# Performance work log

Hardware: AMD Instinct MI355X
Metric: run time of the kernel (lower is better)

Reference implementation:

```python
import jax, jax.numpy as jnp
import numpy as np

N = 4096
NFEAT = 256
NHID1 = 64
NHID2 = 32
NCLASS = 8
NHEADS = 4
NADJ = 2
ALPHA = 0.2  # leaky relu slope
NEG = -9e15


def setup_inputs() -> dict:
    key = jax.random.key(0)
    ks = jax.random.split(key, 14)
    x = jax.random.normal(ks[0], (N, NFEAT), jnp.float32)
    adj = (jax.random.uniform(ks[1], (NADJ, N, N)) < 0.01).astype(jnp.float32)
    adj = jnp.maximum(adj, jnp.eye(N, dtype=jnp.float32)[None])
    s = 0.05
    W1 = jax.random.normal(ks[2], (NADJ, NHEADS, NFEAT, NHID1), jnp.float32) * s
    a1 = jax.random.normal(ks[3], (NADJ, NHEADS, 2, NHID1), jnp.float32) * s
    W2 = jax.random.normal(ks[4], (NADJ, NHEADS, NHID1, NHID2), jnp.float32) * s
    a2 = jax.random.normal(ks[5], (NADJ, NHEADS, 2, NHID2), jnp.float32) * s
    Wi1 = jax.random.normal(ks[6], (NHID1 * NHEADS, NHID1), jnp.float32) * s
    bi1 = jnp.zeros((NHID1,), jnp.float32)
    Wi2 = jax.random.normal(ks[7], (NHID2 * NHEADS, NCLASS), jnp.float32) * s
    bi2 = jnp.zeros((NCLASS,), jnp.float32)
    Wf = jax.random.normal(ks[8], (NCLASS * NADJ, NCLASS), jnp.float32) * s
    bf = jnp.zeros((NCLASS,), jnp.float32)
    return {"x": x, "adj": adj, "W1": W1, "a1": a1, "W2": W2, "a2": a2,
            "Wi1": Wi1, "bi1": bi1, "Wi2": Wi2, "bi2": bi2, "Wf": Wf, "bf": bf}


def gat_multihead(x, adj_i, W, a):
    # x: [n, f]; adj_i: [n, n]; W: [h, f, o]; a: [h, 2, o]
    Wh = jnp.einsum('nf,hfo->hno', x, W)                 # [h, n, o]
    f_src = jnp.einsum('hno,ho->hn', Wh, a[:, 0])        # [h, n]
    f_dst = jnp.einsum('hno,ho->hn', Wh, a[:, 1])        # [h, n]
    e = jax.nn.leaky_relu(f_src[:, :, None] + f_dst[:, None, :], ALPHA)
    e = jnp.where(adj_i[None] > 0, e, NEG)               # masked scores [h, n, n]
    att = jax.nn.softmax(e, axis=-1)
    h = jnp.einsum('hnm,hmo->hno', att, Wh)              # aggregate
    h = jax.nn.elu(h)                                     # concat=True -> elu
    n = x.shape[0]
    return jnp.transpose(h, (1, 0, 2)).reshape(n, -1)     # [n, h*o]


def reference(x, adj, W1, a1, W2, a2, Wi1, bi1, Wi2, bi2, Wf, bf):
    outs = []
    for i in range(NADJ):  # small fixed loop over adjacency graphs
        xi = gat_multihead(x, adj[i], W1[i], a1[i])
        xi = jax.nn.elu(xi @ Wi1 + bi1)
        xi = gat_multihead(xi, adj[i], W2[i], a2[i])
        xi = jax.nn.elu(xi @ Wi2 + bi2)
        outs.append(xi)
    out = jnp.concatenate(outs, axis=1) @ Wf + bf         # [n, nclass]
    l1_loss = jnp.mean(jnp.abs(Wf))
    return jax.nn.log_softmax(out, axis=1), l1_loss
```

## Files before the change

kernel.cpp:

```cpp
#include <hip/hip_runtime.h>
#include <hip/hip_bf16.h>

#define NN 4096
#define NFEAT 256
#define NHID1 64
#define NHID2 32
#define NCLASS 8
#define NHEADS 4
#define NADJ 2
#define CAP 128

template <int KDIM, int NDIM, int RPTY, int ACT, int COEF>
__device__ __forceinline__ void gemm_body(
    const float* __restrict__ A, const float* __restrict__ B,
    const float* __restrict__ bias, float* __restrict__ C,
    const float* __restrict__ ag, float* __restrict__ fsrc,
    float* __restrict__ fdst, const int row0b,
    float* __restrict__ sA, float* __restrict__ sB) {
  constexpr int KT = 32;
  constexpr int TX = NDIM / 4;
  constexpr int TY = 256 / TX;
  constexpr int BR = TY * RPTY;
  constexpr int LDA = BR + 4;
  constexpr int LDB = NDIM + 4;
  const int tid = threadIdx.x;
  const int tx = tid % TX, ty = tid / TX;
  const int c0 = tx * 4;
  float acc[RPTY][4];
#pragma unroll
  for (int i = 0; i < RPTY; ++i)
#pragma unroll
    for (int j = 0; j < 4; ++j) acc[i][j] = 0.f;

  for (int kt = 0; kt < KDIM; kt += KT) {
    __syncthreads();
    for (int i = tid; i < BR * (KT / 4); i += 256) {
      const int r = i / (KT / 4), e = i % (KT / 4);
      const float4 v = *(const float4*)(A + (size_t)(row0b + r) * KDIM + kt + e * 4);
      sA[(e * 4 + 0) * LDA + r] = v.x;
      sA[(e * 4 + 1) * LDA + r] = v.y;
      sA[(e * 4 + 2) * LDA + r] = v.z;
      sA[(e * 4 + 3) * LDA + r] = v.w;
    }
    for (int i = tid; i < KT * (NDIM / 4); i += 256) {
      const int k = i / (NDIM / 4), cc = i % (NDIM / 4);
      *(float4*)&sB[k * LDB + cc * 4] = *(const float4*)(B + (size_t)(kt + k) * NDIM + cc * 4);
    }
    __syncthreads();
#pragma unroll
    for (int k = 0; k < KT; ++k) {
      float a4[RPTY];
      if constexpr (RPTY == 4) {
        const float4 t = *(const float4*)&sA[k * LDA + ty * 4];
        a4[0] = t.x; a4[1] = t.y; a4[2] = t.z; a4[3] = t.w;
      } else {
        const float2 t = *(const float2*)&sA[k * LDA + ty * 2];
        a4[0] = t.x; a4[1] = t.y;
      }
      const float4 bv = *(const float4*)&sB[k * LDB + c0];
      const float b4[4] = {bv.x, bv.y, bv.z, bv.w};
#pragma unroll
      for (int i = 0; i < RPTY; ++i)
#pragma unroll
        for (int j = 0; j < 4; ++j) acc[i][j] += a4[i] * b4[j];
    }
  }
  float b4[4] = {0.f, 0.f, 0.f, 0.f};
  if (bias) {
    const float4 bb = *(const float4*)&bias[c0];
    b4[0] = bb.x; b4[1] = bb.y; b4[2] = bb.z; b4[3] = bb.w;
  }
#pragma unroll
  for (int i = 0; i < RPTY; ++i) {
    const int row = row0b + ty * RPTY + i;
    float4 o;
    float* op = (float*)&o;
#pragma unroll
    for (int j = 0; j < 4; ++j) {
      float v = acc[i][j] + b4[j];
      if (ACT == 1) v = v > 0.f ? v : (__expf(v) - 1.f);
      op[j] = v;
    }
    *(float4*)&C[(size_t)row * NDIM + c0] = o;
  }
  if constexpr (COEF) {
    float aS[4], aD[4];
#pragma unroll
    for (int j = 0; j < 4; ++j) { aS[j] = ag[c0 + j]; aD[j] = ag[NDIM + c0 + j]; }
#pragma unroll
    for (int i = 0; i < RPTY; ++i) {
      float s = 0.f, d = 0.f;
#pragma unroll
      for (int j = 0; j < 4; ++j) { s += acc[i][j] * aS[j]; d += acc[i][j] * aD[j]; }
#pragma unroll
      for (int off = TX / 2; off; off >>= 1) {
        s += __shfl_xor(s, off);
        d += __shfl_xor(d, off);
      }
      if (tx == 0) {
        const int row = row0b + ty * RPTY + i;
        fsrc[row] = s;
        fdst[row] = d;
      }
    }
  }
}

__global__ __launch_bounds__(256) void k1_gemm_edges(
    const float* __restrict__ x, const float* __restrict__ W1,
    const float* __restrict__ a1, float* __restrict__ Wh1,
    float* __restrict__ fs1, float* __restrict__ fd1,
    const float* __restrict__ adj, int* __restrict__ eidx,
    int* __restrict__ ecnt) {
  __shared__ float sA[32 * (64 + 4)];
  __shared__ float sB[32 * (64 + 4)];
  constexpr int NB_GEMM = (NN / 64) * NHEADS * NADJ;
  if (blockIdx.x < NB_GEMM) {
    int b = blockIdx.x;
    const int tile = b % (NN / 64); b /= (NN / 64);
    const int h = b % NHEADS;
    const int g = b / NHEADS;
    const int gh = g * NHEADS + h;
    gemm_body<NFEAT, NHID1, 4, 0, 1>(
        x, W1 + (size_t)gh * NFEAT * NHID1, nullptr,
        Wh1 + (size_t)gh * NN * NHID1, a1 + (size_t)gh * 2 * NHID1,
        fs1 + (size_t)gh * NN, fd1 + (size_t)gh * NN, tile * 64, sA, sB);
  } else {
    const int wave = threadIdx.x >> 6;
    const int lane = threadIdx.x & 63;
    const int r = (blockIdx.x - NB_GEMM) * 4 + wave;
    const float4* row = (const float4*)(adj + (size_t)r * NN);
    int* out = eidx + (size_t)r * CAP;
    int base = 0;
    for (int c = 0; c < NN; c += 256) {
      const float4 v = row[(c >> 2) + lane];
      const int j0 = c + lane * 4;
      const float vt[4] = {v.x, v.y, v.z, v.w};
#pragma unroll
      for (int t = 0; t < 4; ++t) {
        const bool hit = vt[t] > 0.f;
        const unsigned long long m = __ballot(hit);
        if (hit) {
          const int pos = base + __popcll(m & ((1ull << lane) - 1ull));
          if (pos < CAP) out[pos] = j0 + t;
        }
        base += __popcll(m);
      }
    }
    if (lane == 0) ecnt[r] = base < CAP ? base : CAP;
  }
}

template <int KDIM, int NDIM, int RPTY, int ACT, int COEF>
__global__ __launch_bounds__(256) void gemm_tile(
    const float* __restrict__ A, const float* __restrict__ B,
    const float* __restrict__ bias, float* __restrict__ C,
    const float* __restrict__ av, float* __restrict__ fsrc,
    float* __restrict__ fdst,
    size_t asG, size_t bsH, size_t bsG, size_t csH, size_t csG) {
  constexpr int TX = NDIM / 4;
  constexpr int TY = 256 / TX;
  constexpr int BR = TY * RPTY;
  __shared__ float sA[32 * (BR + 4)];
  __shared__ float sB[32 * (NDIM + 4)];
  const int g = blockIdx.z, h = blockIdx.y;
  const int gh = g * NHEADS + h;
  gemm_body<KDIM, NDIM, RPTY, ACT, COEF>(
      A + (size_t)g * asG, B + (size_t)g * bsG + (size_t)h * bsH, bias,
      C + (size_t)g * csG + (size_t)h * csH,
      COEF ? av + (size_t)gh * 2 * NDIM : nullptr,
      COEF ? fsrc + (size_t)gh * NN : nullptr,
      COEF ? fdst + (size_t)gh * NN : nullptr,
      (int)blockIdx.x * BR, sA, sB);
}

#define GATHER(ACC, JJ)                                                     \
  do {                                                                      \
    const float w_ = wgt[wave][JJ];                                         \
    const float4 v_ = *(const float4*)(Wh + (size_t)midx[wave][JJ] * O + c4); \
    ACC.x += w_ * v_.x; ACC.y += w_ * v_.y;                                 \
    ACC.z += w_ * v_.z; ACC.w += w_ * v_.w;                                 \
  } while (0)

template <int O>
__global__ __launch_bounds__(256) void aggregate(const float* __restrict__ Wh,
                                                 const float* __restrict__ fsrc,
                                                 const float* __restrict__ fdst,
                                                 const int* __restrict__ eidx,
                                                 const int* __restrict__ ecnt,
                                                 float* __restrict__ Hout) {
  constexpr int CPL = O / 4;
  constexpr int EPW = 64 / CPL;
  __shared__ float wgt[4][CAP];
  __shared__ int midx[4][CAP];
  const int wave = threadIdx.x >> 6;
  const int lane = threadIdx.x & 63;
  const int n = blockIdx.x * 4 + wave;
  const int h = blockIdx.y, g = blockIdx.z;
  const int gh = g * NHEADS + h;
  Wh += (size_t)gh * NN * O;
  const int cnt = ecnt[(size_t)g * NN + n];
  const int* ei = eidx + (size_t)(g * NN + n) * CAP;
  const float fs = fsrc[(size_t)gh * NN + n];
  const float* fd = fdst + (size_t)gh * NN;
  float mx = -3.4e38f;
  for (int j = lane; j < cnt; j += 64) {
    const int m = ei[j];
    float e = fs + fd[m];
    e = e > 0.f ? e : 0.2f * e;
    midx[wave][j] = m;
    wgt[wave][j] = e;
    mx = fmaxf(mx, e);
  }
  for (int off = 32; off; off >>= 1) mx = fmaxf(mx, __shfl_xor(mx, off));
  float sm = 0.f;
  for (int j = lane; j < cnt; j += 64) {
    const float w = __expf(wgt[wave][j] - mx);
    wgt[wave][j] = w;
    sm += w;
  }
  for (int off = 32; off; off >>= 1) sm += __shfl_xor(sm, off);
  const int sub = lane / CPL;
  const int c4 = (lane % CPL) * 4;
  float4 a0 = {0, 0, 0, 0}, a1 = {0, 0, 0, 0}, a2 = {0, 0, 0, 0}, a3 = {0, 0, 0, 0};
  int j = sub;
  for (; j + 3 * EPW < cnt; j += 4 * EPW) {
    GATHER(a0, j);
    GATHER(a1, j + EPW);
    GATHER(a2, j + 2 * EPW);
    GATHER(a3, j + 3 * EPW);
  }
  for (; j < cnt; j += EPW) GATHER(a0, j);
  float4 acc;
  acc.x = (a0.x + a1.x) + (a2.x + a3.x);
  acc.y = (a0.y + a1.y) + (a2.y + a3.y);
  acc.z = (a0.z + a1.z) + (a2.z + a3.z);
  acc.w = (a0.w + a1.w) + (a2.w + a3.w);
#pragma unroll
  for (int off = CPL; off < 64; off <<= 1) {
    acc.x += __shfl_xor(acc.x, off);
    acc.y += __shfl_xor(acc.y, off);
    acc.z += __shfl_xor(acc.z, off);
    acc.w += __shfl_xor(acc.w, off);
  }
  if (lane < CPL) {
    const float inv = 1.f / sm;
    float4 o;
    o.x = acc.x * inv; o.y = acc.y * inv; o.z = acc.z * inv; o.w = acc.w * inv;
    o.x = o.x > 0.f ? o.x : (__expf(o.x) - 1.f);
    o.y = o.y > 0.f ? o.y : (__expf(o.y) - 1.f);
    o.z = o.z > 0.f ? o.z : (__expf(o.z) - 1.f);
    o.w = o.w > 0.f ? o.w : (__expf(o.w) - 1.f);
    *(float4*)&Hout[(size_t)g * NN * (NHEADS * O) + (size_t)n * (NHEADS * O) +
                    h * O + c4] = o;
  }
}

__global__ __launch_bounds__(256) void tail_fused(const float* __restrict__ h2,
                                                  const float* __restrict__ Wi2,
                                                  const float* __restrict__ bi2,
                                                  const float* __restrict__ Wf,
                                                  const float* __restrict__ bfv,
                                                  float* __restrict__ out) {
  constexpr int K = NHEADS * NHID2;
  __shared__ float A0[16][K + 4];
  __shared__ float A1[16][K + 4];
  __shared__ float Bs[K][NCLASS];
  __shared__ float WfS[2 * NCLASS][NCLASS];
  __shared__ float cat[16][2 * NCLASS + 1];
  const int tid = threadIdx.x;
  const int row0 = blockIdx.x * 16;
  for (int i = tid; i < 16 * (K / 4); i += 256) {
    const int r = i >> 5, e = i & 31;
    *(float4*)&A0[r][e * 4] = *(const float4*)(h2 + (size_t)(row0 + r) * K + e * 4);
    *(float4*)&A1[r][e * 4] =
        *(const float4*)(h2 + (size_t)NN * K + (size_t)(row0 + r) * K + e * 4);
  }
  ((float4*)Bs)[tid] = ((const float4*)Wi2)[tid];
  if (tid < 32) ((float4*)WfS)[tid] = ((const float4*)Wf)[tid];
  __syncthreads();
  const int c = tid & 7;
  const int kk = (tid >> 3) & 1;
  const int r = tid >> 4;
  float s0 = kk ? 0.f : bi2[c], s1 = kk ? 0.f : bi2[c];
#pragma unroll 8
  for (int k = kk * (K / 2); k < (kk + 1) * (K / 2); ++k) {
    s0 += A0[r][k] * Bs[k][c];
    s1 += A1[r][k] * Bs[k][c];
  }
  s0 += __shfl_xor(s0, 8);
  s1 += __shfl_xor(s1, 8);
  if (kk == 0) {
    cat[r][c] = s0 > 0.f ? s0 : (__expf(s0) - 1.f);
    cat[r][NCLASS + c] = s1 > 0.f ? s1 : (__expf(s1) - 1.f);
  }
  __syncthreads();
  float logit = bfv[c];
#pragma unroll
  for (int k = 0; k < 2 * NCLASS; ++k) logit += cat[r][k] * WfS[k][c];
  float m = logit;
#pragma unroll
  for (int off = 4; off; off >>= 1) m = fmaxf(m, __shfl_xor(m, off));
  float s = __expf(logit - m);
#pragma unroll
  for (int off = 4; off; off >>= 1) s += __shfl_xor(s, off);
  if (kk == 0) out[(size_t)(row0 + r) * NCLASS + c] = logit - (logf(s) + m);
  if (blockIdx.x == 0 && tid < 64) {
    float v = fabsf(Wf[tid]) + fabsf(Wf[64 + tid]);
    for (int off = 32; off; off >>= 1) v += __shfl_xor(v, off);
    if (tid == 0) out[NN * NCLASS] = v * (1.f / (2 * NCLASS * NCLASS));
  }
}

extern "C" void kernel_launch(void* const* d_in, const int* in_sizes, int n_in,
                              void* d_out, int out_size, void* d_ws, size_t ws_size,
                              hipStream_t stream) {
  const float* x = (const float*)d_in[0];
  const float* adj = (const float*)d_in[1];
  const float* W1 = (const float*)d_in[2];
  const float* a1 = (const float*)d_in[3];
  const float* W2 = (const float*)d_in[4];
  const float* a2 = (const float*)d_in[5];
  const float* Wi1 = (const float*)d_in[6];
  const float* bi1 = (const float*)d_in[7];
  const float* Wi2 = (const float*)d_in[8];
  const float* bi2 = (const float*)d_in[9];
  const float* Wf = (const float*)d_in[10];
  const float* bfv = (const float*)d_in[11];
  float* out = (float*)d_out;

  char* ws = (char*)d_ws;
  int* eidx = (int*)ws;     ws += (size_t)NADJ * NN * CAP * 4;
  int* ecnt = (int*)ws;     ws += (size_t)NADJ * NN * 4;
  float* Wh1 = (float*)ws;  ws += (size_t)NADJ * NHEADS * NN * NHID1 * 4;
  float* fs1 = (float*)ws;  ws += (size_t)NADJ * NHEADS * NN * 4;
  float* fd1 = (float*)ws;  ws += (size_t)NADJ * NHEADS * NN * 4;
  float* h1 = (float*)ws;   ws += (size_t)NADJ * NN * NHEADS * NHID1 * 4;
  float* x1 = (float*)ws;   ws += (size_t)NADJ * NN * NHID1 * 4;
  float* Wh2 = (float*)ws;  ws += (size_t)NADJ * NHEADS * NN * NHID2 * 4;
  float* fs2 = (float*)ws;  ws += (size_t)NADJ * NHEADS * NN * 4;
  float* fd2 = (float*)ws;  ws += (size_t)NADJ * NHEADS * NN * 4;
  float* h2 = (float*)ws;   ws += (size_t)NADJ * NN * NHEADS * NHID2 * 4;

  k1_gemm_edges<<<512 + NADJ * NN / 4, 256, 0, stream>>>(
      x, W1, a1, Wh1, fs1, fd1, adj, eidx, ecnt);

  aggregate<NHID1><<<dim3(NN / 4, NHEADS, NADJ), 256, 0, stream>>>(
      Wh1, fs1, fd1, eidx, ecnt, h1);

  gemm_tile<NHEADS * NHID1, NHID1, 2, 1, 0><<<dim3(NN / 32, 1, NADJ), 256, 0, stream>>>(
      h1, Wi1, bi1, x1, nullptr, nullptr, nullptr,
      (size_t)NN * NHEADS * NHID1, 0, 0, 0, (size_t)NN * NHID1);

  gemm_tile<NHID1, NHID2, 4, 0, 1><<<dim3(NN / 128, NHEADS, NADJ), 256, 0, stream>>>(
      x1, W2, nullptr, Wh2, a2, fs2, fd2,
      (size_t)NN * NHID1, (size_t)NHID1 * NHID2, (size_t)NHEADS * NHID1 * NHID2,
      (size_t)NN * NHID2, (size_t)NHEADS * NN * NHID2);

  aggregate<NHID2><<<dim3(NN / 4, NHEADS, NADJ), 256, 0, stream>>>(
      Wh2, fs2, fd2, eidx, ecnt, h2);

  tail_fused<<<NN / 16, 256, 0, stream>>>(h2, Wi2, bi2, Wf, bfv, out);
}
```

Before: 101.3 us.

## Fuse layer-1 aggregation with both GEMMs, and layer-2 aggregation with the tail

Cuts the pipeline from six launches to three. Layer-1 attention aggregation, the Wi1 projection with ELU, and the W2 projection plus attention coefficients now run in one kernel over 16-row tiles held in shared memory. Layer-2 aggregation for both graphs is fused with the Wi2/Wf tail and log-softmax. This removes the h1, x1 and h2 round trips through global memory and several launch gaps. In exchange, each wave loops over rows and heads serially, the grids are smaller, and k2 uses a large amount of shared memory, so occupancy and parallelism drop.

```diff
diff --git a/kernel.cpp b/kernel.cpp
--- a/kernel.cpp
+++ b/kernel.cpp
@@ -10,12 +10,11 @@
 #define NADJ 2
 #define CAP 128
 
-template <int KDIM, int NDIM, int RPTY, int ACT, int COEF>
+template <int KDIM, int NDIM, int RPTY>
 __device__ __forceinline__ void gemm_body(
     const float* __restrict__ A, const float* __restrict__ B,
-    const float* __restrict__ bias, float* __restrict__ C,
-    const float* __restrict__ ag, float* __restrict__ fsrc,
-    float* __restrict__ fdst, const int row0b,
+    float* __restrict__ C, const float* __restrict__ ag,
+    float* __restrict__ fsrc, float* __restrict__ fdst, const int row0b,
     float* __restrict__ sA, float* __restrict__ sB) {
   constexpr int KT = 32;
   constexpr int TX = NDIM / 4;
@@ -49,14 +48,8 @@
     __syncthreads();
 #pragma unroll
     for (int k = 0; k < KT; ++k) {
-      float a4[RPTY];
-      if constexpr (RPTY == 4) {
-        const float4 t = *(const float4*)&sA[k * LDA + ty * 4];
-        a4[0] = t.x; a4[1] = t.y; a4[2] = t.z; a4[3] = t.w;
-      } else {
-        const float2 t = *(const float2*)&sA[k * LDA + ty * 2];
-        a4[0] = t.x; a4[1] = t.y;
-      }
+      const float4 t = *(const float4*)&sA[k * LDA + ty * 4];
+      const float a4[4] = {t.x, t.y, t.z, t.w};
       const float4 bv = *(const float4*)&sB[k * LDB + c0];
       const float b4[4] = {bv.x, bv.y, bv.z, bv.w};
 #pragma unroll
@@ -64,44 +57,31 @@
 #pragma unroll
         for (int j = 0; j < 4; ++j) acc[i][j] += a4[i] * b4[j];
     }
-  }
-  float b4[4] = {0.f, 0.f, 0.f, 0.f};
-  if (bias) {
-    const float4 bb = *(const float4*)&bias[c0];
-    b4[0] = bb.x; b4[1] = bb.y; b4[2] = bb.z; b4[3] = bb.w;
   }
 #pragma unroll
   for (int i = 0; i < RPTY; ++i) {
     const int row = row0b + ty * RPTY + i;
     float4 o;
-    float* op = (float*)&o;
-#pragma unroll
-    for (int j = 0; j < 4; ++j) {
-      float v = acc[i][j] + b4[j];
-      if (ACT == 1) v = v > 0.f ? v : (__expf(v) - 1.f);
-      op[j] = v;
-    }
+    o.x = acc[i][0]; o.y = acc[i][1]; o.z = acc[i][2]; o.w = acc[i][3];
     *(float4*)&C[(size_t)row * NDIM + c0] = o;
   }
-  if constexpr (COEF) {
-    float aS[4], aD[4];
-#pragma unroll
-    for (int j = 0; j < 4; ++j) { aS[j] = ag[c0 + j]; aD[j] = ag[NDIM + c0 + j]; }
-#pragma unroll
-    for (int i = 0; i < RPTY; ++i) {
-      float s = 0.f, d = 0.f;
-#pragma unroll
-      for (int j = 0; j < 4; ++j) { s += acc[i][j] * aS[j]; d += acc[i][j] * aD[j]; }
-#pragma unroll
-      for (int off = TX / 2; off; off >>= 1) {
-        s += __shfl_xor(s, off);
-        d += __shfl_xor(d, off);
-      }
-      if (tx == 0) {
-        const int row = row0b + ty * RPTY + i;
-        fsrc[row] = s;
-        fdst[row] = d;
-      }
+  float aS[4], aD[4];
+#pragma unroll
+  for (int j = 0; j < 4; ++j) { aS[j] = ag[c0 + j]; aD[j] = ag[NDIM + c0 + j]; }
+#pragma unroll
+  for (int i = 0; i < RPTY; ++i) {
+    float s = 0.f, d = 0.f;
+#pragma unroll
+    for (int j = 0; j < 4; ++j) { s += acc[i][j] * aS[j]; d += acc[i][j] * aD[j]; }
+#pragma unroll
+    for (int off = TX / 2; off; off >>= 1) {
+      s += __shfl_xor(s, off);
+      d += __shfl_xor(d, off);
+    }
+    if (tx == 0) {
+      const int row = row0b + ty * RPTY + i;
+      fsrc[row] = s;
+      fdst[row] = d;
     }
   }
 }
@@ -121,10 +101,10 @@
     const int h = b % NHEADS;
     const int g = b / NHEADS;
     const int gh = g * NHEADS + h;
-    gemm_body<NFEAT, NHID1, 4, 0, 1>(
-        x, W1 + (size_t)gh * NFEAT * NHID1, nullptr,
-        Wh1 + (size_t)gh * NN * NHID1, a1 + (size_t)gh * 2 * NHID1,
-        fs1 + (size_t)gh * NN, fd1 + (size_t)gh * NN, tile * 64, sA, sB);
+    gemm_body<NFEAT, NHID1, 4>(
+        x, W1 + (size_t)gh * NFEAT * NHID1, Wh1 + (size_t)gh * NN * NHID1,
+        a1 + (size_t)gh * 2 * NHID1, fs1 + (size_t)gh * NN,
+        fd1 + (size_t)gh * NN, tile * 64, sA, sB);
   } else {
     const int wave = threadIdx.x >> 6;
     const int lane = threadIdx.x & 63;
@@ -151,164 +131,259 @@
   }
 }
 
-template <int KDIM, int NDIM, int RPTY, int ACT, int COEF>
-__global__ __launch_bounds__(256) void gemm_tile(
-    const float* __restrict__ A, const float* __restrict__ B,
-    const float* __restrict__ bias, float* __restrict__ C,
-    const float* __restrict__ av, float* __restrict__ fsrc,
-    float* __restrict__ fdst,
-    size_t asG, size_t bsH, size_t bsG, size_t csH, size_t csG) {
-  constexpr int TX = NDIM / 4;
-  constexpr int TY = 256 / TX;
-  constexpr int BR = TY * RPTY;
-  __shared__ float sA[32 * (BR + 4)];
-  __shared__ float sB[32 * (NDIM + 4)];
-  const int g = blockIdx.z, h = blockIdx.y;
-  const int gh = g * NHEADS + h;
-  gemm_body<KDIM, NDIM, RPTY, ACT, COEF>(
-      A + (size_t)g * asG, B + (size_t)g * bsG + (size_t)h * bsH, bias,
-      C + (size_t)g * csG + (size_t)h * csH,
-      COEF ? av + (size_t)gh * 2 * NDIM : nullptr,
-      COEF ? fsrc + (size_t)gh * NN : nullptr,
-      COEF ? fdst + (size_t)gh * NN : nullptr,
-      (int)blockIdx.x * BR, sA, sB);
-}
-
-#define GATHER(ACC, JJ)                                                     \
-  do {                                                                      \
-    const float w_ = wgt[wave][JJ];                                         \
-    const float4 v_ = *(const float4*)(Wh + (size_t)midx[wave][JJ] * O + c4); \
-    ACC.x += w_ * v_.x; ACC.y += w_ * v_.y;                                 \
-    ACC.z += w_ * v_.z; ACC.w += w_ * v_.w;                                 \
-  } while (0)
-
-template <int O>
-__global__ __launch_bounds__(256) void aggregate(const float* __restrict__ Wh,
-                                                 const float* __restrict__ fsrc,
-                                                 const float* __restrict__ fdst,
-                                                 const int* __restrict__ eidx,
-                                                 const int* __restrict__ ecnt,
-                                                 float* __restrict__ Hout) {
-  constexpr int CPL = O / 4;
-  constexpr int EPW = 64 / CPL;
+__global__ __launch_bounds__(256) void k2_fused(
+    const float* __restrict__ Wh1, const float* __restrict__ fs1,
+    const float* __restrict__ fd1, const int* __restrict__ eidx,
+    const int* __restrict__ ecnt, const float* __restrict__ Wi1,
+    const float* __restrict__ bi1, const float* __restrict__ W2,
+    const float* __restrict__ a2, float* __restrict__ Wh2,
+    float* __restrict__ fs2, float* __restrict__ fd2) {
+  __shared__ float h1row[16][256];
+  __shared__ float stage[8192];
+  __shared__ float x1row[16][68];
   __shared__ float wgt[4][CAP];
   __shared__ int midx[4][CAP];
+  const int g = blockIdx.y;
+  const int n0 = blockIdx.x * 16;
   const int wave = threadIdx.x >> 6;
   const int lane = threadIdx.x & 63;
-  const int n = blockIdx.x * 4 + wave;
-  const int h = blockIdx.y, g = blockIdx.z;
-  const int gh = g * NHEADS + h;
-  Wh += (size_t)gh * NN * O;
-  const int cnt = ecnt[(size_t)g * NN + n];
-  const int* ei = eidx + (size_t)(g * NN + n) * CAP;
-  const float fs = fsrc[(size_t)gh * NN + n];
-  const float* fd = fdst + (size_t)gh * NN;
-  float mx = -3.4e38f;
-  for (int j = lane; j < cnt; j += 64) {
-    const int m = ei[j];
-    float e = fs + fd[m];
-    e = e > 0.f ? e : 0.2f * e;
-    midx[wave][j] = m;
-    wgt[wave][j] = e;
-    mx = fmaxf(mx, e);
-  }
-  for (int off = 32; off; off >>= 1) mx = fmaxf(mx, __shfl_xor(mx, off));
-  float sm = 0.f;
-  for (int j = lane; j < cnt; j += 64) {
-    const float w = __expf(wgt[wave][j] - mx);
-    wgt[wave][j] = w;
-    sm += w;
-  }
-  for (int off = 32; off; off >>= 1) sm += __shfl_xor(sm, off);
-  const int sub = lane / CPL;
-  const int c4 = (lane % CPL) * 4;
-  float4 a0 = {0, 0, 0, 0}, a1 = {0, 0, 0, 0}, a2 = {0, 0, 0, 0}, a3 = {0, 0, 0, 0};
-  int j = sub;
-  for (; j + 3 * EPW < cnt; j += 4 * EPW) {
-    GATHER(a0, j);
-    GATHER(a1, j + EPW);
-    GATHER(a2, j + 2 * EPW);
-    GATHER(a3, j + 3 * EPW);
-  }
-  for (; j < cnt; j += EPW) GATHER(a0, j);
-  float4 acc;
-  acc.x = (a0.x + a1.x) + (a2.x + a3.x);
-  acc.y = (a0.y + a1.y) + (a2.y + a3.y);
-  acc.z = (a0.z + a1.z) + (a2.z + a3.z);
-  acc.w = (a0.w + a1.w) + (a2.w + a3.w);
-#pragma unroll
-  for (int off = CPL; off < 64; off <<= 1) {
-    acc.x += __shfl_xor(acc.x, off);
-    acc.y += __shfl_xor(acc.y, off);
-    acc.z += __shfl_xor(acc.z, off);
-    acc.w += __shfl_xor(acc.w, off);
-  }
-  if (lane < CPL) {
-    const float inv = 1.f / sm;
-    float4 o;
-    o.x = acc.x * inv; o.y = acc.y * inv; o.z = acc.z * inv; o.w = acc.w * inv;
-    o.x = o.x > 0.f ? o.x : (__expf(o.x) - 1.f);
-    o.y = o.y > 0.f ? o.y : (__expf(o.y) - 1.f);
-    o.z = o.z > 0.f ? o.z : (__expf(o.z) - 1.f);
-    o.w = o.w > 0.f ? o.w : (__expf(o.w) - 1.f);
-    *(float4*)&Hout[(size_t)g * NN * (NHEADS * O) + (size_t)n * (NHEADS * O) +
-                    h * O + c4] = o;
+
+  for (int rr = 0; rr < 4; ++rr) {
+    const int r = wave * 4 + rr;
+    const int n = n0 + r;
+    const int cnt = ecnt[g * NN + n];
+    const int* ei = eidx + (size_t)(g * NN + n) * CAP;
+    for (int j = lane; j < cnt; j += 64) midx[wave][j] = ei[j];
+    for (int h = 0; h < 4; ++h) {
+      const int gh = g * NHEADS + h;
+      const float fsv = fs1[(size_t)gh * NN + n];
+      const float* fdv = fd1 + (size_t)gh * NN;
+      float mx = -3.4e38f;
+      for (int j = lane; j < cnt; j += 64) {
+        float e = fsv + fdv[midx[wave][j]];
+        e = e > 0.f ? e : 0.2f * e;
+        wgt[wave][j] = e;
+        mx = fmaxf(mx, e);
+      }
+      for (int off = 32; off; off >>= 1) mx = fmaxf(mx, __shfl_xor(mx, off));
+      float sm = 0.f;
+      for (int j = lane; j < cnt; j += 64) {
+        const float w = __expf(wgt[wave][j] - mx);
+        wgt[wave][j] = w;
+        sm += w;
+      }
+      for (int off = 32; off; off >>= 1) sm += __shfl_xor(sm, off);
+      const float* WhH = Wh1 + (size_t)gh * NN * NHID1;
+      const int sub = lane >> 4;
+      const int c4 = (lane & 15) * 4;
+      float4 a0 = {0, 0, 0, 0}, a1v = {0, 0, 0, 0}, a2v = {0, 0, 0, 0}, a3 = {0, 0, 0, 0};
+#define GAT1(ACC, JJ)                                                        \
+  {                                                                          \
+    const float w_ = wgt[wave][JJ];                                          \
+    const float4 v_ = *(const float4*)(WhH + (size_t)midx[wave][JJ] * NHID1 + c4); \
+    ACC.x += w_ * v_.x; ACC.y += w_ * v_.y; ACC.z += w_ * v_.z; ACC.w += w_ * v_.w; \
+  }
+      int j = sub;
+      for (; j + 12 < cnt; j += 16) {
+        GAT1(a0, j); GAT1(a1v, j + 4); GAT1(a2v, j + 8); GAT1(a3, j + 12);
+      }
+      for (; j < cnt; j += 4) GAT1(a0, j);
+#undef GAT1
+      float4 acc;
+      acc.x = (a0.x + a1v.x) + (a2v.x + a3.x);
+      acc.y = (a0.y + a1v.y) + (a2v.y + a3.y);
+      acc.z = (a0.z + a1v.z) + (a2v.z + a3.z);
+      acc.w = (a0.w + a1v.w) + (a2v.w + a3.w);
+#pragma unroll
+      for (int off = 16; off < 64; off <<= 1) {
+        acc.x += __shfl_xor(acc.x, off);
+        acc.y += __shfl_xor(acc.y, off);
+        acc.z += __shfl_xor(acc.z, off);
+        acc.w += __shfl_xor(acc.w, off);
+      }
+      if (lane < 16) {
+        const float inv = 1.f / sm;
+        float4 o;
+        o.x = acc.x * inv; o.y = acc.y * inv; o.z = acc.z * inv; o.w = acc.w * inv;
+        o.x = o.x > 0.f ? o.x : (__expf(o.x) - 1.f);
+        o.y = o.y > 0.f ? o.y : (__expf(o.y) - 1.f);
+        o.z = o.z > 0.f ? o.z : (__expf(o.z) - 1.f);
+        o.w = o.w > 0.f ? o.w : (__expf(o.w) - 1.f);
+        *(float4*)&h1row[r][h * NHID1 + c4] = o;
+      }
+    }
+  }
+
+  const int cB = threadIdx.x & 63;
+  const int rgB = threadIdx.x >> 6;
+  float accB[4] = {0.f, 0.f, 0.f, 0.f};
+  for (int kt = 0; kt < 4; ++kt) {
+    __syncthreads();
+    const float4* src = (const float4*)(Wi1 + kt * 64 * 64);
+    for (int i = threadIdx.x; i < 1024; i += 256) ((float4*)stage)[i] = src[i];
+    __syncthreads();
+    for (int k = 0; k < 64; ++k) {
+      const float b = stage[k * 64 + cB];
+#pragma unroll
+      for (int i = 0; i < 4; ++i) accB[i] += h1row[rgB * 4 + i][kt * 64 + k] * b;
+    }
+  }
+  const float bb = bi1[cB];
+#pragma unroll
+  for (int i = 0; i < 4; ++i) {
+    float v = accB[i] + bb;
+    x1row[rgB * 4 + i][cB] = v > 0.f ? v : (__expf(v) - 1.f);
+  }
+
+  __syncthreads();
+  const float4* w2src = (const float4*)(W2 + (size_t)g * NHEADS * NHID1 * NHID2);
+  for (int i = threadIdx.x; i < 2048; i += 256) ((float4*)stage)[i] = w2src[i];
+  __syncthreads();
+  const int r3 = threadIdx.x >> 4;
+  const int h3 = (threadIdx.x >> 2) & 3;
+  const int c8q = threadIdx.x & 3;
+  const int c8 = c8q * 8;
+  const int gh3 = g * NHEADS + h3;
+  float accC[8] = {0.f, 0.f, 0.f, 0.f, 0.f, 0.f, 0.f, 0.f};
+  for (int k = 0; k < 64; ++k) {
+    const float av = x1row[r3][k];
+#pragma unroll
+    for (int j = 0; j < 8; ++j) accC[j] += av * stage[(h3 * 64 + k) * 32 + c8 + j];
+  }
+  float4 o0, o1;
+  o0.x = accC[0]; o0.y = accC[1]; o0.z = accC[2]; o0.w = accC[3];
+  o1.x = accC[4]; o1.y = accC[5]; o1.z = accC[6]; o1.w = accC[7];
+  float* wp = Wh2 + ((size_t)gh3 * NN + n0 + r3) * NHID2 + c8;
+  *(float4*)wp = o0;
+  *(float4*)(wp + 4) = o1;
+  const float* aaS = a2 + ((size_t)gh3 * 2) * NHID2 + c8;
+  const float* aaD = aaS + NHID2;
+  float s = 0.f, d = 0.f;
+#pragma unroll
+  for (int j = 0; j < 8; ++j) { s += accC[j] * aaS[j]; d += accC[j] * aaD[j]; }
+  s += __shfl_xor(s, 1); s += __shfl_xor(s, 2);
+  d += __shfl_xor(d, 1); d += __shfl_xor(d, 2);
+  if (c8q == 0) {
+    fs2[(size_t)gh3 * NN + n0 + r3] = s;
+    fd2[(size_t)gh3 * NN + n0 + r3] = d;
   }
 }
 
-__global__ __launch_bounds__(256) void tail_fused(const float* __restrict__ h2,
-                                                  const float* __restrict__ Wi2,
-                                                  const float* __restrict__ bi2,
-                                                  const float* __restrict__ Wf,
-                                                  const float* __restrict__ bfv,
-                                                  float* __restrict__ out) {
-  constexpr int K = NHEADS * NHID2;
-  __shared__ float A0[16][K + 4];
-  __shared__ float A1[16][K + 4];
-  __shared__ float Bs[K][NCLASS];
-  __shared__ float WfS[2 * NCLASS][NCLASS];
-  __shared__ float cat[16][2 * NCLASS + 1];
-  const int tid = threadIdx.x;
-  const int row0 = blockIdx.x * 16;
-  for (int i = tid; i < 16 * (K / 4); i += 256) {
-    const int r = i >> 5, e = i & 31;
-    *(float4*)&A0[r][e * 4] = *(const float4*)(h2 + (size_t)(row0 + r) * K + e * 4);
-    *(float4*)&A1[r][e * 4] =
-        *(const float4*)(h2 + (size_t)NN * K + (size_t)(row0 + r) * K + e * 4);
-  }
-  ((float4*)Bs)[tid] = ((const float4*)Wi2)[tid];
-  if (tid < 32) ((float4*)WfS)[tid] = ((const float4*)Wf)[tid];
+__global__ __launch_bounds__(256) void k3_fused(
+    const float* __restrict__ Wh2, const float* __restrict__ fs2,
+    const float* __restrict__ fd2, const int* __restrict__ eidx,
+    const int* __restrict__ ecnt, const float* __restrict__ Wi2,
+    const float* __restrict__ bi2, const float* __restrict__ Wf,
+    const float* __restrict__ bfv, float* __restrict__ out) {
+  __shared__ float h2cat[8][260];
+  __shared__ float Wi2s[128 * 8];
+  __shared__ float WfS[16 * 8];
+  __shared__ float cat[8][17];
+  __shared__ float wgt[4][CAP];
+  __shared__ int midx[4][CAP];
+  const int n0 = blockIdx.x * 8;
+  const int wave = threadIdx.x >> 6;
+  const int lane = threadIdx.x & 63;
+  const int g = wave >> 1;
+
+  for (int i = threadIdx.x; i < 256; i += 256) ((float4*)Wi2s)[i] = ((const float4*)Wi2)[i];
+  if (threadIdx.x < 32) ((float4*)WfS)[threadIdx.x] = ((const float4*)Wf)[threadIdx.x];
+
+  for (int rr = 0; rr < 4; ++rr) {
+    const int r = (wave & 1) * 4 + rr;
+    const int n = n0 + r;
+    const int cnt = ecnt[g * NN + n];
+    const int* ei = eidx + (size_t)(g * NN + n) * CAP;
+    for (int j = lane; j < cnt; j += 64) midx[wave][j] = ei[j];
+    for (int h = 0; h < 4; ++h) {
+      const int gh = g * NHEADS + h;
+      const float fsv = fs2[(size_t)gh * NN + n];
+      const float* fdv = fd2 + (size_t)gh * NN;
+      float mx = -3.4e38f;
+      for (int j = lane; j < cnt; j += 64) {
+        float e = fsv + fdv[midx[wave][j]];
+        e = e > 0.f ? e : 0.2f * e;
+        wgt[wave][j] = e;
+        mx = fmaxf(mx, e);
+      }
+      for (int off = 32; off; off >>= 1) mx = fmaxf(mx, __shfl_xor(mx, off));
+      float sm = 0.f;
+      for (int j = lane; j < cnt; j += 64) {
+        const float w = __expf(wgt[wave][j] - mx);
+        wgt[wave][j] = w;
+        sm += w;
+      }
+      for (int off = 32; off; off >>= 1) sm += __shfl_xor(sm, off);
+      const float* WhH = Wh2 + (size_t)gh * NN * NHID2;
+      const int sub = lane >> 3;
+      const int c4 = (lane & 7) * 4;
+      float4 a0 = {0, 0, 0, 0}, a1v = {0, 0, 0, 0}, a2v = {0, 0, 0, 0}, a3 = {0, 0, 0, 0};
+#define GAT2(ACC, JJ)                                                        \
+  {                                                                          \
+    const float w_ = wgt[wave][JJ];                                          \
+    const float4 v_ = *(const float4*)(WhH + (size_t)midx[wave][JJ] * NHID2 + c4); \
+    ACC.x += w_ * v_.x; ACC.y += w_ * v_.y; ACC.z += w_ * v_.z; ACC.w += w_ * v_.w; \
+  }
+      int j = sub;
+      for (; j + 24 < cnt; j += 32) {
+        GAT2(a0, j); GAT2(a1v, j + 8); GAT2(a2v, j + 16); GAT2(a3, j + 24);
+      }
+      for (; j < cnt; j += 8) GAT2(a0, j);
+#undef GAT2
+      float4 acc;
+      acc.x = (a0.x + a1v.x) + (a2v.x + a3.x);
+      acc.y = (a0.y + a1v.y) + (a2v.y + a3.y);
+      acc.z = (a0.z + a1v.z) + (a2v.z + a3.z);
+      acc.w = (a0.w + a1v.w) + (a2v.w + a3.w);
+#pragma unroll
+      for (int off = 8; off < 64; off <<= 1) {
+        acc.x += __shfl_xor(acc.x, off);
+        acc.y += __shfl_xor(acc.y, off);
+        acc.z += __shfl_xor(acc.z, off);
+        acc.w += __shfl_xor(acc.w, off);
+      }
+      if (lane < 8) {
+        const float inv = 1.f / sm;
+        float4 o;
+        o.x = acc.x * inv; o.y = acc.y * inv; o.z = acc.z * inv; o.w = acc.w * inv;
+        o.x = o.x > 0.f ? o.x : (__expf(o.x) - 1.f);
+        o.y = o.y > 0.f ? o.y : (__expf(o.y) - 1.f);
+        o.z = o.z > 0.f ? o.z : (__expf(o.z) - 1.f);
+        o.w = o.w > 0.f ? o.w : (__expf(o.w) - 1.f);
+        *(float4*)&h2cat[r][g * 128 + h * NHID2 + c4] = o;
+      }
+    }
+  }
   __syncthreads();
-  const int c = tid & 7;
-  const int kk = (tid >> 3) & 1;
-  const int r = tid >> 4;
-  float s0 = kk ? 0.f : bi2[c], s1 = kk ? 0.f : bi2[c];
-#pragma unroll 8
-  for (int k = kk * (K / 2); k < (kk + 1) * (K / 2); ++k) {
-    s0 += A0[r][k] * Bs[k][c];
-    s1 += A1[r][k] * Bs[k][c];
-  }
-  s0 += __shfl_xor(s0, 8);
-  s1 += __shfl_xor(s1, 8);
-  if (kk == 0) {
-    cat[r][c] = s0 > 0.f ? s0 : (__expf(s0) - 1.f);
-    cat[r][NCLASS + c] = s1 > 0.f ? s1 : (__expf(s1) - 1.f);
+
+  if (threadIdx.x < 128) {
+    const int r = threadIdx.x >> 4;
+    const int gg = (threadIdx.x >> 3) & 1;
+    const int c = threadIdx.x & 7;
+    float s = bi2[c];
+    for (int k = 0; k < 128; ++k) s += h2cat[r][gg * 128 + k] * Wi2s[k * 8 + c];
+    cat[r][gg * 8 + c] = s > 0.f ? s : (__expf(s) - 1.f);
   }
   __syncthreads();
-  float logit = bfv[c];
-#pragma unroll
-  for (int k = 0; k < 2 * NCLASS; ++k) logit += cat[r][k] * WfS[k][c];
-  float m = logit;
-#pragma unroll
-  for (int off = 4; off; off >>= 1) m = fmaxf(m, __shfl_xor(m, off));
-  float s = __expf(logit - m);
-#pragma unroll
-  for (int off = 4; off; off >>= 1) s += __shfl_xor(s, off);
-  if (kk == 0) out[(size_t)(row0 + r) * NCLASS + c] = logit - (logf(s) + m);
-  if (blockIdx.x == 0 && tid < 64) {
-    float v = fabsf(Wf[tid]) + fabsf(Wf[64 + tid]);
+
+  if (threadIdx.x < 64) {
+    const int r = threadIdx.x >> 3;
+    const int c = threadIdx.x & 7;
+    float logit = bfv[c];
+#pragma unroll
+    for (int k = 0; k < 16; ++k) logit += cat[r][k] * WfS[k * 8 + c];
+    float m = logit;
+#pragma unroll
+    for (int off = 4; off; off >>= 1) m = fmaxf(m, __shfl_xor(m, off));
+    float s = __expf(logit - m);
+#pragma unroll
+    for (int off = 4; off; off >>= 1) s += __shfl_xor(s, off);
+    out[(size_t)(n0 + r) * NCLASS + c] = logit - (logf(s) + m);
+  }
+  if (blockIdx.x == 0 && threadIdx.x < 64) {
+    float v = fabsf(Wf[threadIdx.x]) + fabsf(Wf[64 + threadIdx.x]);
     for (int off = 32; off; off >>= 1) v += __shfl_xor(v, off);
-    if (tid == 0) out[NN * NCLASS] = v * (1.f / (2 * NCLASS * NCLASS));
+    if (threadIdx.x == 0) out[NN * NCLASS] = v * (1.f / (2 * NCLASS * NCLASS));
   }
 }
 
@@ -335,30 +410,16 @@
   float* Wh1 = (float*)ws;  ws += (size_t)NADJ * NHEADS * NN * NHID1 * 4;
   float* fs1 = (float*)ws;  ws += (size_t)NADJ * NHEADS * NN * 4;
   float* fd1 = (float*)ws;  ws += (size_t)NADJ * NHEADS * NN * 4;
-  float* h1 = (float*)ws;   ws += (size_t)NADJ * NN * NHEADS * NHID1 * 4;
-  float* x1 = (float*)ws;   ws += (size_t)NADJ * NN * NHID1 * 4;
   float* Wh2 = (float*)ws;  ws += (size_t)NADJ * NHEADS * NN * NHID2 * 4;
   float* fs2 = (float*)ws;  ws += (size_t)NADJ * NHEADS * NN * 4;
   float* fd2 = (float*)ws;  ws += (size_t)NADJ * NHEADS * NN * 4;
-  float* h2 = (float*)ws;   ws += (size_t)NADJ * NN * NHEADS * NHID2 * 4;
 
   k1_gemm_edges<<<512 + NADJ * NN / 4, 256, 0, stream>>>(
       x, W1, a1, Wh1, fs1, fd1, adj, eidx, ecnt);
 
-  aggregate<NHID1><<<dim3(NN / 4, NHEADS, NADJ), 256, 0, stream>>>(
-      Wh1, fs1, fd1, eidx, ecnt, h1);
-
-  gemm_tile<NHEADS * NHID1, NHID1, 2, 1, 0><<<dim3(NN / 32, 1, NADJ), 256, 0, stream>>>(
-      h1, Wi1, bi1, x1, nullptr, nullptr, nullptr,
-      (size_t)NN * NHEADS * NHID1, 0, 0, 0, (size_t)NN * NHID1);
-
-  gemm_tile<NHID1, NHID2, 4, 0, 1><<<dim3(NN / 128, NHEADS, NADJ), 256, 0, stream>>>(
-      x1, W2, nullptr, Wh2, a2, fs2, fd2,
-      (size_t)NN * NHID1, (size_t)NHID1 * NHID2, (size_t)NHEADS * NHID1 * NHID2,
-      (size_t)NN * NHID2, (size_t)NHEADS * NN * NHID2);
-
-  aggregate<NHID2><<<dim3(NN / 4, NHEADS, NADJ), 256, 0, stream>>>(
-      Wh2, fs2, fd2, eidx, ecnt, h2);
-
-  tail_fused<<<NN / 16, 256, 0, stream>>>(h2, Wi2, bi2, Wf, bfv, out);
+  k2_fused<<<dim3(NN / 16, NADJ), 256, 0, stream>>>(
+      Wh1, fs1, fd1, eidx, ecnt, Wi1, bi1, W2, a2, Wh2, fs2, fd2);
+
+  k3_fused<<<NN / 8, 256, 0, stream>>>(
+      Wh2, fs2, fd2, eidx, ecnt, Wi2, bi2, Wf, bfv, out);
 }
```

Result: slower. 151.2 us (+49.3%).
